# Optimization experiments

Hardware: AMD Instinct MI355X
Metric: run time of the kernel (lower is better)

The kernel has to match this reference:

```python
import jax, jax.numpy as jnp
import numpy as np

D = 768      # embedding_dim
M = 3072     # mlp_dim
G = 4        # num_expert_groups
E = 8        # experts_per_group
KG = 2       # k_groups
KE = 4       # k_experts
EPS = 1e-6   # gate weight threshold from the torch module


def setup_inputs() -> dict:
    key = jax.random.key(0)
    ks = jax.random.split(key, 9)
    x = jax.random.normal(ks[0], (1, 1024, D), dtype=jnp.float32)
    Wg = jax.random.normal(ks[1], (D, G), dtype=jnp.float32) * 0.02
    bg = jax.random.normal(ks[2], (G,), dtype=jnp.float32) * 0.01
    We = jax.random.normal(ks[3], (G, D, E), dtype=jnp.float32) * 0.02
    be = jax.random.normal(ks[4], (G, E), dtype=jnp.float32) * 0.01
    W1 = jax.random.normal(ks[5], (G, E, D, M), dtype=jnp.float32) * 0.02
    b1 = jax.random.normal(ks[6], (G, E, M), dtype=jnp.float32) * 0.01
    W2 = jax.random.normal(ks[7], (G, E, M, D), dtype=jnp.float32) * 0.02
    b2 = jax.random.normal(ks[8], (G, E, D), dtype=jnp.float32) * 0.01
    return {"x": x, "Wg": Wg, "bg": bg, "We": We, "be": be,
            "W1": W1, "b1": b1, "W2": W2, "b2": b2}


def _topk_gates(logits, k):
    # top-k logits -> softmax over the k entries, then zero out weights < 1e-6
    top, idx = jax.lax.top_k(logits, k)
    gates = jax.nn.softmax(top, axis=-1)
    gates = jnp.where(gates >= EPS, gates, jnp.zeros_like(gates))
    return gates, idx


def reference(x, Wg, bg, We, be, W1, b1, W2, b2):
    orig_shape = x.shape
    xf = x.reshape(-1, D)  # [N, D]

    # ---- level 1: group gating (eval mode: clean logits, no noise) ----
    glog = xf @ Wg + bg                      # [N, G]
    ggates, gidx = _topk_gates(glog, KG)     # [N, KG]
    gw = jnp.einsum('nk,nkg->ng', ggates,
                    jax.nn.one_hot(gidx, G, dtype=xf.dtype))  # dense [N, G]

    # ---- level 2: expert gating within each group ----
    # computed densely for all groups; unselected groups get zero group weight
    elog = jnp.einsum('nd,gde->nge', xf, We) + be  # [N, G, E]
    egates, eidx = _topk_gates(elog, KE)            # [N, G, KE]
    ew = jnp.einsum('ngk,ngke->nge', egates,
                    jax.nn.one_hot(eidx, E, dtype=xf.dtype))  # dense [N, G, E]

    combine = gw[:, :, None] * ew  # [N, G, E] combine weights

    # ---- expert MLPs (dense compute, combine-weighted sum) ----
    y = jnp.zeros_like(xf)
    for g in range(G):  # small fixed loop over expert groups
        h = jax.nn.gelu(jnp.einsum('nd,edm->enm', xf, W1[g]) + b1[g][:, None, :],
                        approximate=False)               # [E, N, M]
        o = jnp.einsum('enm,emd->end', h, W2[g]) + b2[g][:, None, :]  # [E, N, D]
        y = y + jnp.einsum('end,ne->nd', o, combine[:, g, :])
    return y.reshape(orig_shape)
```

## Files before the change

### kernel.cpp

```cpp
#include <hip/hip_runtime.h>
#include <hip/hip_bf16.h>
#include <math.h>

#define NTOK 1024
#define DDIM 768
#define MDIM 3072
#define GN 4
#define EN 8
#define NEXP 32
#define NPAIR 8192
#define EPSW 1e-6f
#define MAXRB 96

typedef __attribute__((ext_vector_type(4))) float f32x4;
typedef __attribute__((ext_vector_type(4))) int   i32x4;
typedef __attribute__((ext_vector_type(4))) unsigned short u16x4;
typedef __attribute__((ext_vector_type(8))) __bf16 bf16x8;

__device__ __forceinline__ unsigned short f2bf(float f) {
  unsigned u = __builtin_bit_cast(unsigned, f);
  u += 0x7FFFu + ((u >> 16) & 1u);
  return (unsigned short)(u >> 16);
}

__global__ void init_kernel(int* __restrict__ p) { p[threadIdx.x] = 0; }

__global__ __launch_bounds__(256) void zero_y(float* __restrict__ y) {
  ((f32x4*)y)[blockIdx.x * 256 + threadIdx.x] = (f32x4){0.f, 0.f, 0.f, 0.f};
}

__global__ __launch_bounds__(256) void x2bf(const float* __restrict__ x,
                                            unsigned short* __restrict__ xb) {
  const int i = (blockIdx.x * 256 + threadIdx.x) * 16;
#pragma unroll
  for (int j = 0; j < 4; ++j) {
    const f32x4 v = *(const f32x4*)(x + i + j * 4);
    u16x4 p = { f2bf(v.x), f2bf(v.y), f2bf(v.z), f2bf(v.w) };
    *(u16x4*)(xb + i + j * 4) = p;
  }
}

__global__ __launch_bounds__(256) void gating_kernel(
    const float* __restrict__ x, const float* __restrict__ Wg,
    const float* __restrict__ bg, const float* __restrict__ We,
    const float* __restrict__ be, int* __restrict__ counts,
    int* __restrict__ pair_e, float* __restrict__ pair_w)
{
  __shared__ float xr[DDIM];
  __shared__ float logits[36];
  const int n = blockIdx.x;
  const int tid = threadIdx.x;
  const float* xp = x + (size_t)n * DDIM;
  for (int d = tid; d < DDIM; d += 256) xr[d] = xp[d];
  __syncthreads();

  const int w = tid >> 6, lane = tid & 63;
  for (int j = 0; j < 9; ++j) {
    const int o = w + 4 * j;
    float s = 0.f;
    if (o < 4) {
      for (int d = lane; d < DDIM; d += 64) s += xr[d] * Wg[d * GN + o];
    } else {
      const int g = (o - 4) >> 3, e = (o - 4) & 7;
      const float* wp = We + (size_t)g * DDIM * EN + e;
      for (int d = lane; d < DDIM; d += 64) s += xr[d] * wp[d * EN];
    }
    for (int off = 32; off; off >>= 1) s += __shfl_xor(s, off);
    if (lane == 0) logits[o] = s + ((o < 4) ? bg[o] : be[o - 4]);
  }
  __syncthreads();

  if (tid == 0) {
    float gl[4];
    for (int i = 0; i < 4; ++i) gl[i] = logits[i];
    int i0 = 0;
    for (int i = 1; i < 4; ++i) if (gl[i] > gl[i0]) i0 = i;
    int i1 = -1;
    for (int i = 0; i < 4; ++i) {
      if (i == i0) continue;
      if (i1 < 0 || gl[i] > gl[i1]) i1 = i;
    }
    const float m = gl[i0];
    const float e1 = expf(gl[i1] - m);
    const float s2 = 1.f + e1;
    float gv[2] = { 1.f / s2, e1 / s2 };
    int gi[2] = { i0, i1 };
    for (int r = 0; r < 2; ++r) if (gv[r] < EPSW) gv[r] = 0.f;

    for (int r = 0; r < 2; ++r) {
      const int g = gi[r];
      float el[8];
      for (int e = 0; e < 8; ++e) el[e] = logits[4 + g * 8 + e];
      int sel[4];
      for (int q = 0; q < 4; ++q) {
        int best = -1;
        for (int e = 0; e < 8; ++e) {
          bool used = false;
          for (int p = 0; p < q; ++p) if (sel[p] == e) used = true;
          if (used) continue;
          if (best < 0 || el[e] > el[best]) best = e;
        }
        sel[q] = best;
      }
      const float mm = el[sel[0]];
      float ex[4]; float ss = 0.f;
      for (int q = 0; q < 4; ++q) { ex[q] = expf(el[sel[q]] - mm); ss += ex[q]; }
      for (int q = 0; q < 4; ++q) {
        float ew = ex[q] / ss;
        if (ew < EPSW) ew = 0.f;
        const int gbl = g * 8 + sel[q];
        const int j = r * 4 + q;
        pair_e[n * 8 + j] = gbl;
        pair_w[n * 8 + j] = gv[r] * ew;
        atomicAdd(&counts[gbl], 1);
      }
    }
  }
}

__global__ void scan_kernel(const int* __restrict__ counts, int* __restrict__ offsets,
                            int* __restrict__ rb_ge, int* __restrict__ rb_by,
                            int* __restrict__ nrb)
{
  if (threadIdx.x == 0) {
    int a = 0, n = 0;
    for (int e = 0; e < NEXP; ++e) {
      offsets[e] = a;
      const int c = counts[e];
      a += c;
      for (int b = 0; b * 128 < c; ++b) { rb_ge[n] = e; rb_by[n] = b; ++n; }
    }
    *nrb = n;
  }
}

__global__ __launch_bounds__(256) void scatter_kernel(
    const int* __restrict__ pair_e, const float* __restrict__ pair_w,
    const int* __restrict__ offsets, int* __restrict__ cursor,
    int* __restrict__ slot_tok, float* __restrict__ slot_w)
{
  const int idx = blockIdx.x * 256 + threadIdx.x;
  if (idx < NPAIR) {
    const int e = pair_e[idx];
    const int s = offsets[e] + atomicAdd(&cursor[e], 1);
    slot_tok[s] = idx >> 3;
    slot_w[s] = pair_w[idx];
  }
}

template<int K, int NLD, int EPI, int GATHER, int KS>
__global__ __launch_bounds__(256, 2) void moe_gemm_fl(
    const unsigned short* __restrict__ Abase, const float* __restrict__ W,
    const float* __restrict__ bias, const int* __restrict__ counts,
    const int* __restrict__ offsets, const float* __restrict__ slot_w,
    const int* __restrict__ slot_tok, const int* __restrict__ rb_ge,
    const int* __restrict__ rb_by, const int* __restrict__ nrb,
    unsigned short* __restrict__ Hout, float* __restrict__ Yout)
{
  constexpr int KC = K / KS;
  constexpr int NT = KC / 32;
  constexpr int BUFB = 16384;

  const int rb = blockIdx.x;
  if (rb >= *nrb) return;
  const int ge = rb_ge[rb];
  const int by = rb_by[rb];
  const int cnt = counts[ge];
  const int off = offsets[ge];
  const int nb = blockIdx.y;
  const int ks = (KS > 1) ? blockIdx.z : 0;
  const int kbase = ks * KC;
  const int tid = threadIdx.x;

  __shared__ __align__(16) unsigned char lds[2 * BUFB];

  const int am = tid >> 2, ac = tid & 3;
  const int asw0 = am * 64 + ((ac ^ ((am ^ (am >> 2)) & 3)) * 16);
  const int asw1 = asw0 + 4096;

  const int kq = tid >> 5, ln = tid & 31;
  const float* bp = W + (size_t)ge * K * NLD + (size_t)(kbase + kq * 4) * NLD
                      + nb * 128 + ln;
  int bwr[4];
#pragma unroll
  for (int ii = 0; ii < 4; ++ii) {
    const int n = ln + 32 * ii;
    const int s = (n ^ (n >> 2)) & 3;
    bwr[ii] = 8192 + n * 64 + (((kq >> 1) ^ s) * 16) + ((kq & 1) * 8);
  }

  const int w = tid >> 6, lane = tid & 63;
  const int wr = (w >> 1) * 64, wc = (w & 1) * 64;
  const int l15 = lane & 15, l4 = lane >> 4;
  int aoff[4], boff[4];
#pragma unroll
  for (int mf = 0; mf < 4; ++mf) {
    const int m = wr + mf * 16 + l15;
    aoff[mf] = m * 64 + ((l4 ^ ((m ^ (m >> 2)) & 3)) * 16);
  }
#pragma unroll
  for (int nf = 0; nf < 4; ++nf) {
    const int n = wc + nf * 16 + l15;
    boff[nf] = 8192 + n * 64 + ((l4 ^ ((n ^ (n >> 2)) & 3)) * 16);
  }

  int gr0 = by * 128 + am;      if (gr0 >= cnt) gr0 = cnt - 1;
  int gr1 = by * 128 + am + 64; if (gr1 >= cnt) gr1 = cnt - 1;
  const unsigned short* ap0;
  const unsigned short* ap1;
  if (GATHER) {
    ap0 = Abase + (size_t)slot_tok[off + gr0] * K + kbase + ac * 8;
    ap1 = Abase + (size_t)slot_tok[off + gr1] * K + kbase + ac * 8;
  } else {
    ap0 = Abase + (size_t)(off + gr0) * K + kbase + ac * 8;
    ap1 = Abase + (size_t)(off + gr1) * K + kbase + ac * 8;
  }

  f32x4 acc[4][4];
#pragma unroll
  for (int mf = 0; mf < 4; ++mf)
#pragma unroll
    for (int nf = 0; nf < 4; ++nf)
      acc[mf][nf] = (f32x4){0.f, 0.f, 0.f, 0.f};

  i32x4 aA0, aA1, aB0, aB1, aC0, aC1;
  float bA[16], bB[16], bC[16];

#define LOADA(T, R0, R1) { \
    R0 = *(const i32x4*)(ap0 + (T) * 32); \
    R1 = *(const i32x4*)(ap1 + (T) * 32); }
#define LOADB(T, BS) { _Pragma("unroll") \
    for (int ii = 0; ii < 4; ++ii) { _Pragma("unroll") \
      for (int jj = 0; jj < 4; ++jj) \
        BS[ii * 4 + jj] = bp[(size_t)((T) * 32 + jj) * NLD + 32 * ii]; } }
#define CVTW(R0, R1, BS, BASE) { \
    *(i32x4*)((BASE) + asw0) = R0; \
    *(i32x4*)((BASE) + asw1) = R1; \
    _Pragma("unroll") \
    for (int ii = 0; ii < 4; ++ii) { \
      u16x4 p = { f2bf(BS[ii*4+0]), f2bf(BS[ii*4+1]), f2bf(BS[ii*4+2]), f2bf(BS[ii*4+3]) }; \
      *(u16x4*)((BASE) + bwr[ii]) = p; } }
#define COMPUTE(BASE) { bf16x8 afr[4], bfr[4]; _Pragma("unroll") \
    for (int mf = 0; mf < 4; ++mf) \
      afr[mf] = __builtin_bit_cast(bf16x8, *(const i32x4*)((BASE) + aoff[mf])); \
    _Pragma("unroll") \
    for (int nf = 0; nf < 4; ++nf) \
      bfr[nf] = __builtin_bit_cast(bf16x8, *(const i32x4*)((BASE) + boff[nf])); \
    _Pragma("unroll") \
    for (int mf = 0; mf < 4; ++mf) { _Pragma("unroll") \
      for (int nf = 0; nf < 4; ++nf) \
        acc[mf][nf] = __builtin_amdgcn_mfma_f32_16x16x32_bf16( \
            afr[mf], bfr[nf], acc[mf][nf], 0, 0, 0); } }
#define STEP(T, C0, C1, CB, I0, I1, IB, BASE) { \
    if ((T) + 2 < NT) { LOADA((T) + 2, I0, I1); LOADB((T) + 2, IB); } \
    CVTW(C0, C1, CB, BASE); \
    asm volatile("s_waitcnt lgkmcnt(0)" ::: "memory"); \
    __builtin_amdgcn_s_barrier(); \
    COMPUTE(BASE); \
  }

  LOADA(0, aA0, aA1); LOADB(0, bA);
  LOADA(1, aB0, aB1); LOADB(1, bB);

  for (int t = 0; t < NT; t += 6) {
    STEP(t + 0, aA0, aA1, bA, aC0, aC1, bC, lds);
    STEP(t + 1, aB0, aB1, bB, aA0, aA1, bA, lds + BUFB);
    STEP(t + 2, aC0, aC1, bC, aB0, aB1, bB, lds);
    STEP(t + 3, aA0, aA1, bA, aC0, aC1, bC, lds + BUFB);
    STEP(t + 4, aB0, aB1, bB, aA0, aA1, bA, lds);
    STEP(t + 5, aC0, aC1, bC, aB0, aB1, bB, lds + BUFB);
  }
#undef LOADA
#undef LOADB
#undef CVTW
#undef COMPUTE
#undef STEP

#pragma unroll
  for (int mf = 0; mf < 4; ++mf) {
    const int rb2 = by * 128 + wr + mf * 16 + l4 * 4;
    if constexpr (EPI == 0) {
#pragma unroll
      for (int nf = 0; nf < 4; ++nf) {
        const int col = nb * 128 + wc + nf * 16 + l15;
        const float bv = bias[(size_t)ge * NLD + col];
#pragma unroll
        for (int j = 0; j < 4; ++j) {
          const int r = rb2 + j;
          if (r < cnt) {
            const float v = acc[mf][nf][j] + bv;
            const float gl = 0.5f * v * (1.f + erff(v * 0.70710678118654752f));
            Hout[(size_t)(off + r) * NLD + col] = f2bf(gl);
          }
        }
      }
    } else {
#pragma unroll
      for (int j = 0; j < 4; ++j) {
        const int r = rb2 + j;
        if (r < cnt) {
          const int slot = off + r;
          const float sw = slot_w[slot];
          const int tok = slot_tok[slot];
#pragma unroll
          for (int nf = 0; nf < 4; ++nf) {
            const int col = nb * 128 + wc + nf * 16 + l15;
            const float bv = (ks == 0) ? bias[(size_t)ge * NLD + col] : 0.f;
            atomicAdd(&Yout[(size_t)tok * DDIM + col], sw * (acc[mf][nf][j] + bv));
          }
        }
      }
    }
  }
}

extern "C" void kernel_launch(void* const* d_in, const int* in_sizes, int n_in,
                              void* d_out, int out_size, void* d_ws, size_t ws_size,
                              hipStream_t stream)
{
  const float* x  = (const float*)d_in[0];
  const float* Wg = (const float*)d_in[1];
  const float* bg = (const float*)d_in[2];
  const float* We = (const float*)d_in[3];
  const float* be = (const float*)d_in[4];
  const float* W1 = (const float*)d_in[5];
  const float* b1 = (const float*)d_in[6];
  const float* W2 = (const float*)d_in[7];
  const float* b2 = (const float*)d_in[8];
  float* y = (float*)d_out;

  char* ws = (char*)d_ws;
  int*   counts   = (int*)(ws + 0);
  int*   offsets  = (int*)(ws + 128);
  int*   cursor   = (int*)(ws + 256);
  int*   nrb      = (int*)(ws + 384);
  int*   rb_ge    = (int*)(ws + 512);
  int*   rb_by    = (int*)(ws + 896);
  int*   pair_e   = (int*)(ws + 2048);
  float* pair_w   = (float*)(ws + 34816);
  int*   slot_tok = (int*)(ws + 67584);
  float* slot_w   = (float*)(ws + 100352);
  unsigned short* xb = (unsigned short*)(ws + 135168);
  unsigned short* H  = (unsigned short*)(ws + 12715008);

  init_kernel<<<1, 256, 0, stream>>>((int*)ws);
  zero_y<<<NTOK * DDIM / 1024, 256, 0, stream>>>(y);
  x2bf<<<NTOK * DDIM / 4096, 256, 0, stream>>>(x, xb);
  gating_kernel<<<NTOK, 256, 0, stream>>>(x, Wg, bg, We, be, counts, pair_e, pair_w);
  scan_kernel<<<1, 64, 0, stream>>>(counts, offsets, rb_ge, rb_by, nrb);
  scatter_kernel<<<NPAIR / 256, 256, 0, stream>>>(pair_e, pair_w, offsets, cursor,
                                                  slot_tok, slot_w);

  moe_gemm_fl<DDIM, MDIM, 0, 1, 1><<<dim3(MAXRB, MDIM / 128, 1), 256, 0, stream>>>(
      xb, W1, b1, counts, offsets, nullptr, slot_tok, rb_ge, rb_by, nrb, H, nullptr);
  moe_gemm_fl<MDIM, DDIM, 1, 0, 4><<<dim3(MAXRB, DDIM / 128, 4), 256, 0, stream>>>(
      H, W2, b2, counts, offsets, slot_w, slot_tok, rb_ge, rb_by, nrb, nullptr, y);
}
```

Baseline: 560.3 us.

## Reshape MoE GEMM tiles to 256x64 with direct global-to-LDS A loads

Changes the expert GEMM tile from 128x128 to 256 rows by 64 columns, so each fp32 weight column slice is read and converted by fewer row-blocks, and rebuilds the row-block list at 256-row granularity. The bf16 activation tile is now loaded with global_load_lds straight into shared memory instead of through registers, and the pipeline becomes a simple double-buffer with prefetch issued after the barrier. Occupancy hint rises to 3 blocks per CU and the second GEMM uses 2 K-splits instead of 4. The risks are more padding waste for experts with small token counts, fewer blocks per launch, and less load latency hiding in the shallower pipeline.

```diff
diff --git a/kernel.cpp b/kernel.cpp
--- a/kernel.cpp
+++ b/kernel.cpp
@@ -10,7 +10,7 @@
 #define NEXP 32
 #define NPAIR 8192
 #define EPSW 1e-6f
-#define MAXRB 96
+#define MAXRB 64
 
 typedef __attribute__((ext_vector_type(4))) float f32x4;
 typedef __attribute__((ext_vector_type(4))) int   i32x4;
@@ -21,6 +21,12 @@
   unsigned u = __builtin_bit_cast(unsigned, f);
   u += 0x7FFFu + ((u >> 16) & 1u);
   return (unsigned short)(u >> 16);
+}
+
+__device__ __forceinline__ void gld_lds16(const void* g, void* l) {
+  __builtin_amdgcn_global_load_lds(
+      (const __attribute__((address_space(1))) void*)g,
+      (__attribute__((address_space(3))) void*)l, 16, 0, 0);
 }
 
 __global__ void init_kernel(int* __restrict__ p) { p[threadIdx.x] = 0; }
@@ -128,7 +134,7 @@
       offsets[e] = a;
       const int c = counts[e];
       a += c;
-      for (int b = 0; b * 128 < c; ++b) { rb_ge[n] = e; rb_by[n] = b; ++n; }
+      for (int b = 0; b * 256 < c; ++b) { rb_ge[n] = e; rb_by[n] = b; ++n; }
     }
     *nrb = n;
   }
@@ -149,7 +155,7 @@
 }
 
 template<int K, int NLD, int EPI, int GATHER, int KS>
-__global__ __launch_bounds__(256, 2) void moe_gemm_fl(
+__global__ __launch_bounds__(256, 3) void moe_gemm_bw(
     const unsigned short* __restrict__ Abase, const float* __restrict__ W,
     const float* __restrict__ bias, const int* __restrict__ counts,
     const int* __restrict__ offsets, const float* __restrict__ slot_w,
@@ -159,7 +165,8 @@
 {
   constexpr int KC = K / KS;
   constexpr int NT = KC / 32;
-  constexpr int BUFB = 16384;
+  constexpr int ABY = 16384;
+  constexpr int BUFB = ABY + 4096;
 
   const int rb = blockIdx.x;
   if (rb >= *nrb) return;
@@ -174,46 +181,40 @@
 
   __shared__ __align__(16) unsigned char lds[2 * BUFB];
 
-  const int am = tid >> 2, ac = tid & 3;
-  const int asw0 = am * 64 + ((ac ^ ((am ^ (am >> 2)) & 3)) * 16);
-  const int asw1 = asw0 + 4096;
+  const unsigned short* asrc[4];
+#pragma unroll
+  for (int i = 0; i < 4; ++i) {
+    const int q = tid + 256 * i;
+    const int m = q >> 2, c = q & 3;
+    const int sc = c ^ ((m ^ (m >> 2)) & 3);
+    int gr = by * 256 + m; if (gr >= cnt) gr = cnt - 1;
+    const int row = GATHER ? slot_tok[off + gr] : (off + gr);
+    asrc[i] = Abase + (size_t)row * K + kbase + sc * 8;
+  }
 
   const int kq = tid >> 5, ln = tid & 31;
   const float* bp = W + (size_t)ge * K * NLD + (size_t)(kbase + kq * 4) * NLD
-                      + nb * 128 + ln;
-  int bwr[4];
-#pragma unroll
-  for (int ii = 0; ii < 4; ++ii) {
+                      + nb * 64 + ln;
+  int bwr[2];
+#pragma unroll
+  for (int ii = 0; ii < 2; ++ii) {
     const int n = ln + 32 * ii;
     const int s = (n ^ (n >> 2)) & 3;
-    bwr[ii] = 8192 + n * 64 + (((kq >> 1) ^ s) * 16) + ((kq & 1) * 8);
+    bwr[ii] = ABY + n * 64 + (((kq >> 1) ^ s) * 16) + ((kq & 1) * 8);
   }
 
   const int w = tid >> 6, lane = tid & 63;
-  const int wr = (w >> 1) * 64, wc = (w & 1) * 64;
   const int l15 = lane & 15, l4 = lane >> 4;
   int aoff[4], boff[4];
 #pragma unroll
   for (int mf = 0; mf < 4; ++mf) {
-    const int m = wr + mf * 16 + l15;
+    const int m = w * 64 + mf * 16 + l15;
     aoff[mf] = m * 64 + ((l4 ^ ((m ^ (m >> 2)) & 3)) * 16);
   }
 #pragma unroll
   for (int nf = 0; nf < 4; ++nf) {
-    const int n = wc + nf * 16 + l15;
-    boff[nf] = 8192 + n * 64 + ((l4 ^ ((n ^ (n >> 2)) & 3)) * 16);
-  }
-
-  int gr0 = by * 128 + am;      if (gr0 >= cnt) gr0 = cnt - 1;
-  int gr1 = by * 128 + am + 64; if (gr1 >= cnt) gr1 = cnt - 1;
-  const unsigned short* ap0;
-  const unsigned short* ap1;
-  if (GATHER) {
-    ap0 = Abase + (size_t)slot_tok[off + gr0] * K + kbase + ac * 8;
-    ap1 = Abase + (size_t)slot_tok[off + gr1] * K + kbase + ac * 8;
-  } else {
-    ap0 = Abase + (size_t)(off + gr0) * K + kbase + ac * 8;
-    ap1 = Abase + (size_t)(off + gr1) * K + kbase + ac * 8;
+    const int n = nf * 16 + l15;
+    boff[nf] = ABY + n * 64 + ((l4 ^ ((n ^ (n >> 2)) & 3)) * 16);
   }
 
   f32x4 acc[4][4];
@@ -223,21 +224,17 @@
     for (int nf = 0; nf < 4; ++nf)
       acc[mf][nf] = (f32x4){0.f, 0.f, 0.f, 0.f};
 
-  i32x4 aA0, aA1, aB0, aB1, aC0, aC1;
-  float bA[16], bB[16], bC[16];
-
-#define LOADA(T, R0, R1) { \
-    R0 = *(const i32x4*)(ap0 + (T) * 32); \
-    R1 = *(const i32x4*)(ap1 + (T) * 32); }
+  float bA[8], bB[8];
+
+#define ISSUE_A(T, BASE) { _Pragma("unroll") \
+    for (int i = 0; i < 4; ++i) \
+      gld_lds16(asrc[i] + (T) * 32, (BASE) + (tid + 256 * i) * 16); }
 #define LOADB(T, BS) { _Pragma("unroll") \
-    for (int ii = 0; ii < 4; ++ii) { _Pragma("unroll") \
+    for (int ii = 0; ii < 2; ++ii) { _Pragma("unroll") \
       for (int jj = 0; jj < 4; ++jj) \
         BS[ii * 4 + jj] = bp[(size_t)((T) * 32 + jj) * NLD + 32 * ii]; } }
-#define CVTW(R0, R1, BS, BASE) { \
-    *(i32x4*)((BASE) + asw0) = R0; \
-    *(i32x4*)((BASE) + asw1) = R1; \
-    _Pragma("unroll") \
-    for (int ii = 0; ii < 4; ++ii) { \
+#define CVTW(BS, BASE) { _Pragma("unroll") \
+    for (int ii = 0; ii < 2; ++ii) { \
       u16x4 p = { f2bf(BS[ii*4+0]), f2bf(BS[ii*4+1]), f2bf(BS[ii*4+2]), f2bf(BS[ii*4+3]) }; \
       *(u16x4*)((BASE) + bwr[ii]) = p; } }
 #define COMPUTE(BASE) { bf16x8 afr[4], bfr[4]; _Pragma("unroll") \
@@ -251,26 +248,28 @@
       for (int nf = 0; nf < 4; ++nf) \
         acc[mf][nf] = __builtin_amdgcn_mfma_f32_16x16x32_bf16( \
             afr[mf], bfr[nf], acc[mf][nf], 0, 0, 0); } }
-#define STEP(T, C0, C1, CB, I0, I1, IB, BASE) { \
-    if ((T) + 2 < NT) { LOADA((T) + 2, I0, I1); LOADB((T) + 2, IB); } \
-    CVTW(C0, C1, CB, BASE); \
+#define STEP(T, CB, IB, BASE, OBASE) { \
+    CVTW(CB, BASE); \
     asm volatile("s_waitcnt lgkmcnt(0)" ::: "memory"); \
     __builtin_amdgcn_s_barrier(); \
+    asm volatile("" ::: "memory"); \
+    if ((T) + 1 < NT) { \
+      ISSUE_A((T) + 1, OBASE); \
+      __builtin_amdgcn_sched_barrier(0); \
+      LOADB((T) + 1, IB); \
+    } \
     COMPUTE(BASE); \
   }
 
-  LOADA(0, aA0, aA1); LOADB(0, bA);
-  LOADA(1, aB0, aB1); LOADB(1, bB);
-
-  for (int t = 0; t < NT; t += 6) {
-    STEP(t + 0, aA0, aA1, bA, aC0, aC1, bC, lds);
-    STEP(t + 1, aB0, aB1, bB, aA0, aA1, bA, lds + BUFB);
-    STEP(t + 2, aC0, aC1, bC, aB0, aB1, bB, lds);
-    STEP(t + 3, aA0, aA1, bA, aC0, aC1, bC, lds + BUFB);
-    STEP(t + 4, aB0, aB1, bB, aA0, aA1, bA, lds);
-    STEP(t + 5, aC0, aC1, bC, aB0, aB1, bB, lds + BUFB);
-  }
-#undef LOADA
+  ISSUE_A(0, lds);
+  __builtin_amdgcn_sched_barrier(0);
+  LOADB(0, bA);
+
+  for (int t = 0; t < NT; t += 2) {
+    STEP(t,     bA, bB, lds,        lds + BUFB);
+    STEP(t + 1, bB, bA, lds + BUFB, lds);
+  }
+#undef ISSUE_A
 #undef LOADB
 #undef CVTW
 #undef COMPUTE
@@ -278,11 +277,11 @@
 
 #pragma unroll
   for (int mf = 0; mf < 4; ++mf) {
-    const int rb2 = by * 128 + wr + mf * 16 + l4 * 4;
+    const int rb2 = by * 256 + w * 64 + mf * 16 + l4 * 4;
     if constexpr (EPI == 0) {
 #pragma unroll
       for (int nf = 0; nf < 4; ++nf) {
-        const int col = nb * 128 + wc + nf * 16 + l15;
+        const int col = nb * 64 + nf * 16 + l15;
         const float bv = bias[(size_t)ge * NLD + col];
 #pragma unroll
         for (int j = 0; j < 4; ++j) {
@@ -304,7 +303,7 @@
           const int tok = slot_tok[slot];
 #pragma unroll
           for (int nf = 0; nf < 4; ++nf) {
-            const int col = nb * 128 + wc + nf * 16 + l15;
+            const int col = nb * 64 + nf * 16 + l15;
             const float bv = (ks == 0) ? bias[(size_t)ge * NLD + col] : 0.f;
             atomicAdd(&Yout[(size_t)tok * DDIM + col], sw * (acc[mf][nf][j] + bv));
           }
@@ -351,8 +350,8 @@
   scatter_kernel<<<NPAIR / 256, 256, 0, stream>>>(pair_e, pair_w, offsets, cursor,
                                                   slot_tok, slot_w);
 
-  moe_gemm_fl<DDIM, MDIM, 0, 1, 1><<<dim3(MAXRB, MDIM / 128, 1), 256, 0, stream>>>(
+  moe_gemm_bw<DDIM, MDIM, 0, 1, 1><<<dim3(MAXRB, MDIM / 64, 1), 256, 0, stream>>>(
       xb, W1, b1, counts, offsets, nullptr, slot_tok, rb_ge, rb_by, nrb, H, nullptr);
-  moe_gemm_fl<MDIM, DDIM, 1, 0, 4><<<dim3(MAXRB, DDIM / 128, 4), 256, 0, stream>>>(
+  moe_gemm_bw<MDIM, DDIM, 1, 0, 2><<<dim3(MAXRB, DDIM / 64, 2), 256, 0, stream>>>(
       H, W2, b2, counts, offsets, slot_w, slot_tok, rb_ge, rb_by, nrb, nullptr, y);
 }
```

New measurement: 589.7 us. +5.3%, slower.
